# Performance work log

Measured on AMD Instinct MI355X. Metric: run time of the kernel, lower is better.

The kernel has to match this reference:

```python
import jax, jax.numpy as jnp
import numpy as np

DIM = 64
SHAPE = (1, DIM, 12, 12, 12)  # B, C, D, H, W


def setup_inputs() -> dict:
    key = jax.random.key(0)
    k1, k2, k3, k4 = jax.random.split(key, 4)
    x = jax.random.normal(k1, SHAPE, dtype=jnp.float32)
    # torch nn.Linear weights: [out, in]; scale like default init
    w_qkv = jax.random.normal(k2, (3 * DIM, DIM), dtype=jnp.float32) * (1.0 / np.sqrt(DIM))
    w_proj = jax.random.normal(k3, (DIM, DIM), dtype=jnp.float32) * (1.0 / np.sqrt(DIM))
    b_proj = jax.random.normal(k4, (DIM,), dtype=jnp.float32) * 0.01
    return {"x": x, "w_qkv": w_qkv, "w_proj": w_proj, "b_proj": b_proj}


def reference(x, w_qkv, w_proj, b_proj):
    B, C, D, H, W = x.shape
    num_heads = C // 2  # head_dim = 2, per module definition
    head_dim = C // num_heads
    scale = head_dim ** (-0.5)
    N = D * H * W

    # [B, N, C] token layout (permute channels last, flatten spatial)
    xt = jnp.transpose(x, (0, 2, 3, 4, 1)).reshape(B, N, C)
    qkv = xt @ w_qkv.T  # [B, N, 3C]
    qkv = qkv.reshape(B, N, 3, num_heads, head_dim).transpose(2, 0, 3, 1, 4)
    q, k, v = qkv[0], qkv[1], qkv[2]  # each [B, h, N, d]

    attn = jnp.einsum('bhqd,bhkd->bhqk', q, k) * scale  # materialized scores
    attn = jax.nn.softmax(attn, axis=-1)
    out = jnp.einsum('bhqk,bhkd->bhqd', attn, v)  # [B, h, N, d]
    out = out.transpose(0, 2, 1, 3).reshape(B, D, H, W, C)
    out = out @ w_proj.T + b_proj  # [B, D, H, W, C]
    return out
```

## Files before the change

### kernel.cpp

```cpp
#include <hip/hip_runtime.h>
#include <hip/hip_bf16.h>

#define N_TOK  1728
#define CDIM   64
#define NHEADS 32
#define QTILES 27
#define SCALE  0.70710678118654752f
#define LOG2E  1.44269504088896340736f
#define JW     8
#define JCHUNK (N_TOK / JW)

__device__ __forceinline__ float ldin(const void* p, int i, int f32) {
    if (f32) return ((const float*)p)[i];
    union { unsigned int b; float f; } c;
    c.b = ((unsigned int)((const unsigned short*)p)[i]) << 16;
    return c.f;
}

__device__ __forceinline__ int sniff_f32(const void* x) {
    union { unsigned int b; float f; } c;
    c.b = ((unsigned int)((const unsigned short*)x)[threadIdx.x & 63]) << 16;
    int bad = (((c.b >> 23) & 0xFF) == 0xFF) || (fabsf(c.f) > 1e10f);
    return (__ballot(bad) != 0ULL) ? 1 : 0;
}

__global__ void __launch_bounds__(512, 4)
attn_fused(const void* __restrict__ xv, const void* __restrict__ wv,
           float* __restrict__ O) {
    __shared__ float4 KVs[N_TOK];
    __shared__ float2 Qs[64];
    __shared__ float  redbuf[JW * 64 * 3];
    const int f    = sniff_f32(xv);
    const int tid  = threadIdx.x;
    const int lane = tid & 63;
    const int wav  = tid >> 6;
    const int h    = blockIdx.x / QTILES;
    const int t0   = (blockIdx.x % QTILES) * 64;

    if (f) {
        if (tid < 432) {
            const float* x   = (const float*)xv;
            const float* w   = (const float*)wv;
            const float* wq0 = w + (2 * h) * CDIM;
            const float* wq1 = w + (2 * h + 1) * CDIM;
            const float* wk0 = w + (64 + 2 * h) * CDIM;
            const float* wk1 = w + (65 + 2 * h) * CDIM;
            const float* wv0 = w + (128 + 2 * h) * CDIM;
            const float* wv1 = w + (129 + 2 * h) * CDIM;
            const int n0 = tid * 4;
            const bool qd = (n0 & ~63) == t0;
            float k0[4] = {0,0,0,0}, k1[4] = {0,0,0,0};
            float v0[4] = {0,0,0,0}, v1[4] = {0,0,0,0};
            float q0[4] = {0,0,0,0}, q1[4] = {0,0,0,0};
            if (qd) {
#pragma unroll 4
                for (int c = 0; c < CDIM; ++c) {
                    const float4 xc = *(const float4*)(x + c * N_TOK + n0);
                    const float sk0 = wk0[c], sk1 = wk1[c];
                    const float sv0 = wv0[c], sv1 = wv1[c];
                    const float sq0 = wq0[c], sq1 = wq1[c];
                    const float xs[4] = {xc.x, xc.y, xc.z, xc.w};
#pragma unroll
                    for (int j = 0; j < 4; ++j) {
                        k0[j] = fmaf(xs[j], sk0, k0[j]);
                        k1[j] = fmaf(xs[j], sk1, k1[j]);
                        v0[j] = fmaf(xs[j], sv0, v0[j]);
                        v1[j] = fmaf(xs[j], sv1, v1[j]);
                        q0[j] = fmaf(xs[j], sq0, q0[j]);
                        q1[j] = fmaf(xs[j], sq1, q1[j]);
                    }
                }
            } else {
#pragma unroll 4
                for (int c = 0; c < CDIM; ++c) {
                    const float4 xc = *(const float4*)(x + c * N_TOK + n0);
                    const float sk0 = wk0[c], sk1 = wk1[c];
                    const float sv0 = wv0[c], sv1 = wv1[c];
                    const float xs[4] = {xc.x, xc.y, xc.z, xc.w};
#pragma unroll
                    for (int j = 0; j < 4; ++j) {
                        k0[j] = fmaf(xs[j], sk0, k0[j]);
                        k1[j] = fmaf(xs[j], sk1, k1[j]);
                        v0[j] = fmaf(xs[j], sv0, v0[j]);
                        v1[j] = fmaf(xs[j], sv1, v1[j]);
                    }
                }
            }
#pragma unroll
            for (int j = 0; j < 4; ++j) {
                KVs[j * 432 + tid] = make_float4(k0[j], k1[j], v0[j], v1[j]);
                if (qd) Qs[n0 + j - t0] = make_float2(q0[j] * (SCALE * LOG2E),
                                                      q1[j] * (SCALE * LOG2E));
            }
        }
    } else {
        for (int n = tid; n < N_TOK; n += 512) {
            float k0 = 0, k1 = 0, v0 = 0, v1 = 0, q0 = 0, q1 = 0;
            for (int c = 0; c < CDIM; ++c) {
                float xc = ldin(xv, c * N_TOK + n, 0);
                q0 = fmaf(xc, ldin(wv, (2 * h) * CDIM + c, 0), q0);
                q1 = fmaf(xc, ldin(wv, (2 * h + 1) * CDIM + c, 0), q1);
                k0 = fmaf(xc, ldin(wv, (64 + 2 * h) * CDIM + c, 0), k0);
                k1 = fmaf(xc, ldin(wv, (65 + 2 * h) * CDIM + c, 0), k1);
                v0 = fmaf(xc, ldin(wv, (128 + 2 * h) * CDIM + c, 0), v0);
                v1 = fmaf(xc, ldin(wv, (129 + 2 * h) * CDIM + c, 0), v1);
            }
            KVs[(n & 3) * 432 + (n >> 2)] = make_float4(k0, k1, v0, v1);
            if ((n & ~63) == t0)
                Qs[n - t0] = make_float2(q0 * (SCALE * LOG2E),
                                         q1 * (SCALE * LOG2E));
        }
    }
    __syncthreads();

    const float2 q = Qs[lane];
    const float4* KVp = &KVs[wav * JCHUNK];
    float la = 0.f, lb = 0.f, oa0 = 0.f, oa1 = 0.f, ob0 = 0.f, ob1 = 0.f;
    for (int g = 0; g < JCHUNK; g += 8) {
        float4 k[8];
#pragma unroll
        for (int u = 0; u < 8; ++u) k[u] = KVp[g + u];
#pragma unroll
        for (int u = 0; u < 8; ++u) {
            float e = __builtin_amdgcn_exp2f(fmaf(q.x, k[u].x, q.y * k[u].y));
            if (u & 1) { lb += e; ob0 = fmaf(e, k[u].z, ob0); ob1 = fmaf(e, k[u].w, ob1); }
            else       { la += e; oa0 = fmaf(e, k[u].z, oa0); oa1 = fmaf(e, k[u].w, oa1); }
        }
    }
    float* red = redbuf + wav * 192 + lane * 3;
    red[0] = la + lb; red[1] = oa0 + ob0; red[2] = oa1 + ob1;
    __syncthreads();
    if (wav == 0) {
        float L = 0.f, A = 0.f, B = 0.f;
#pragma unroll
        for (int w = 0; w < JW; ++w) {
            const float* r = redbuf + w * 192 + lane * 3;
            L += r[0]; A += r[1]; B += r[2];
        }
        float inv = 1.0f / L;
        int n = t0 + lane;
        *((float2*)(O + n * CDIM + 2 * h)) = make_float2(A * inv, B * inv);
    }
}

__global__ void __launch_bounds__(256)
proj_kernel(const void* __restrict__ xv,
            const float* __restrict__ O,
            const void* __restrict__ w_proj, const void* __restrict__ b_proj,
            void* __restrict__ out) {
    __shared__ float Ws[CDIM * 65];
    const int f    = sniff_f32(xv);
    const int tid  = threadIdx.x;
    const int lane = tid & 63;
    const int wav  = tid >> 6;
    for (int e = tid; e < CDIM * CDIM; e += 256)
        Ws[(e & 63) * 65 + (e >> 6)] = ldin(w_proj, e, f);
    __syncthreads();
    int n = blockIdx.x * 4 + wav;
    float acc = ldin(b_proj, lane, f);
#pragma unroll 8
    for (int ci = 0; ci < CDIM; ++ci)
        acc = fmaf(O[n * CDIM + ci],
                   Ws[ci * 65 + lane], acc);
    if (f) ((float*)out)[n * CDIM + lane] = acc;
    else   ((__hip_bfloat16*)out)[n * CDIM + lane] = __float2bfloat16(acc);
}

extern "C" void kernel_launch(void* const* d_in, const int* in_sizes, int n_in,
                              void* d_out, int out_size, void* d_ws, size_t ws_size,
                              hipStream_t stream) {
    const void* x      = d_in[0];
    const void* w_qkv  = d_in[1];
    const void* w_proj = d_in[2];
    const void* b_proj = d_in[3];

    float* O = (float*)d_ws;

    attn_fused <<<NHEADS * QTILES, 512, 0, stream>>>(x, w_qkv, O);
    proj_kernel<<<432, 256, 0, stream>>>(x, O, w_proj, b_proj, d_out);
}
```

Measured before the change: 104.6 us.

## Store K/V and Q as packed fp16 pairs and use fdot2 for scores

Packs K, V and the scaled Q into half-precision pairs in shared memory, so two tokens' K/V fit in one 16-byte LDS load. Scores are computed with the fp16 dot2 builtin instead of separate float FMAs. This halves LDS footprint and read traffic in the inner loop and may raise occupancy. The cost is fp16 rounding of Q/K/V, which adds accuracy risk in the softmax exponent.

```diff
diff --git a/kernel.cpp b/kernel.cpp
--- a/kernel.cpp
+++ b/kernel.cpp
@@ -5,10 +5,26 @@
 #define CDIM   64
 #define NHEADS 32
 #define QTILES 27
+#define NPAIR  (N_TOK / 2)
 #define SCALE  0.70710678118654752f
 #define LOG2E  1.44269504088896340736f
 #define JW     8
-#define JCHUNK (N_TOK / JW)
+#define PCH    (NPAIR / JW)
+
+typedef _Float16 h2 __attribute__((ext_vector_type(2)));
+union H2U { h2 h; unsigned int u; };
+
+__device__ __forceinline__ unsigned int pack2(float a, float b) {
+    H2U c; c.h.x = (_Float16)a; c.h.y = (_Float16)b; return c.u;
+}
+__device__ __forceinline__ float hdot2(unsigned int q, unsigned int k) {
+    H2U a, b; a.u = q; b.u = k;
+#if __has_builtin(__builtin_amdgcn_fdot2)
+    return __builtin_amdgcn_fdot2(a.h, b.h, 0.0f, false);
+#else
+    return fmaf((float)a.h.x, (float)b.h.x, (float)a.h.y * (float)b.h.y);
+#endif
+}
 
 __device__ __forceinline__ float ldin(const void* p, int i, int f32) {
     if (f32) return ((const float*)p)[i];
@@ -16,7 +32,6 @@
     c.b = ((unsigned int)((const unsigned short*)p)[i]) << 16;
     return c.f;
 }
-
 __device__ __forceinline__ int sniff_f32(const void* x) {
     union { unsigned int b; float f; } c;
     c.b = ((unsigned int)((const unsigned short*)x)[threadIdx.x & 63]) << 16;
@@ -27,9 +42,9 @@
 __global__ void __launch_bounds__(512, 4)
 attn_fused(const void* __restrict__ xv, const void* __restrict__ wv,
            float* __restrict__ O) {
-    __shared__ float4 KVs[N_TOK];
-    __shared__ float2 Qs[64];
-    __shared__ float  redbuf[JW * 64 * 3];
+    __shared__ uint4 KVh[NPAIR];
+    __shared__ unsigned int Qs[64];
+    __shared__ float redbuf[JW * 64 * 3];
     const int f    = sniff_f32(xv);
     const int tid  = threadIdx.x;
     const int lane = tid & 63;
@@ -86,14 +101,19 @@
                     }
                 }
             }
-#pragma unroll
-            for (int j = 0; j < 4; ++j) {
-                KVs[j * 432 + tid] = make_float4(k0[j], k1[j], v0[j], v1[j]);
-                if (qd) Qs[n0 + j - t0] = make_float2(q0[j] * (SCALE * LOG2E),
-                                                      q1[j] * (SCALE * LOG2E));
+            KVh[2 * tid]     = make_uint4(pack2(k0[0], k1[0]), pack2(k0[1], k1[1]),
+                                          pack2(v0[0], v1[0]), pack2(v0[1], v1[1]));
+            KVh[2 * tid + 1] = make_uint4(pack2(k0[2], k1[2]), pack2(k0[3], k1[3]),
+                                          pack2(v0[2], v1[2]), pack2(v0[3], v1[3]));
+            if (qd) {
+#pragma unroll
+                for (int j = 0; j < 4; ++j)
+                    Qs[n0 + j - t0] = pack2(q0[j] * (SCALE * LOG2E),
+                                            q1[j] * (SCALE * LOG2E));
             }
         }
     } else {
+        unsigned int* KVu = (unsigned int*)KVh;
         for (int n = tid; n < N_TOK; n += 512) {
             float k0 = 0, k1 = 0, v0 = 0, v1 = 0, q0 = 0, q1 = 0;
             for (int c = 0; c < CDIM; ++c) {
@@ -105,26 +125,31 @@
                 v0 = fmaf(xc, ldin(wv, (128 + 2 * h) * CDIM + c, 0), v0);
                 v1 = fmaf(xc, ldin(wv, (129 + 2 * h) * CDIM + c, 0), v1);
             }
-            KVs[(n & 3) * 432 + (n >> 2)] = make_float4(k0, k1, v0, v1);
+            KVu[(n >> 1) * 4 + (n & 1)]     = pack2(k0, k1);
+            KVu[(n >> 1) * 4 + 2 + (n & 1)] = pack2(v0, v1);
             if ((n & ~63) == t0)
-                Qs[n - t0] = make_float2(q0 * (SCALE * LOG2E),
-                                         q1 * (SCALE * LOG2E));
+                Qs[n - t0] = pack2(q0 * (SCALE * LOG2E), q1 * (SCALE * LOG2E));
         }
     }
     __syncthreads();
 
-    const float2 q = Qs[lane];
-    const float4* KVp = &KVs[wav * JCHUNK];
+    const unsigned int qh = Qs[lane];
+    const uint4* KVp = &KVh[wav * PCH];
     float la = 0.f, lb = 0.f, oa0 = 0.f, oa1 = 0.f, ob0 = 0.f, ob1 = 0.f;
-    for (int g = 0; g < JCHUNK; g += 8) {
-        float4 k[8];
-#pragma unroll
-        for (int u = 0; u < 8; ++u) k[u] = KVp[g + u];
-#pragma unroll
-        for (int u = 0; u < 8; ++u) {
-            float e = __builtin_amdgcn_exp2f(fmaf(q.x, k[u].x, q.y * k[u].y));
-            if (u & 1) { lb += e; ob0 = fmaf(e, k[u].z, ob0); ob1 = fmaf(e, k[u].w, ob1); }
-            else       { la += e; oa0 = fmaf(e, k[u].z, oa0); oa1 = fmaf(e, k[u].w, oa1); }
+    for (int g = 0; g < PCH; g += 4) {
+        uint4 d[4];
+#pragma unroll
+        for (int u = 0; u < 4; ++u) d[u] = KVp[g + u];
+#pragma unroll
+        for (int u = 0; u < 4; ++u) {
+            H2U va, vb; va.u = d[u].z; vb.u = d[u].w;
+            float ea = __builtin_amdgcn_exp2f(hdot2(qh, d[u].x));
+            float eb = __builtin_amdgcn_exp2f(hdot2(qh, d[u].y));
+            la += ea; lb += eb;
+            oa0 = fmaf(ea, (float)va.h.x, oa0);
+            oa1 = fmaf(ea, (float)va.h.y, oa1);
+            ob0 = fmaf(eb, (float)vb.h.x, ob0);
+            ob1 = fmaf(eb, (float)vb.h.y, ob1);
         }
     }
     float* red = redbuf + wav * 192 + lane * 3;
```

Result: no change. 105.9 us (+1.3%).
